# Performance work log

Measured on AMD Instinct MI355X. Metric: run time of the kernel, lower is better.

The kernel has to match this reference:

```python
import jax, jax.numpy as jnp
import numpy as np

IMG = 512
STRIDES = (8.0, 16.0, 32.0)   # p3, p4, p5
ROI = 7                        # roi_size
SR = 2                         # roi_align sampling ratio (fixed; torchvision default -1 is adaptive)
IOU_LOW, IOU_HIGH = 0.4, 0.6   # fg/bg matching thresholds (2nd-stage)
NUM_CLASSES = 20
B, R, M, C = 4, 256, 40, 256


def _make_boxes(key, b, n, max_wh):
    k1, k2 = jax.random.split(key)
    cxy = jax.random.uniform(k1, (b, n, 2), minval=0.0, maxval=float(IMG))
    wh = jax.random.uniform(k2, (b, n, 2), minval=16.0, maxval=float(max_wh))
    x1y1 = jnp.clip(cxy - wh / 2, 0.0, IMG - 1.0)
    x2y2 = jnp.clip(cxy + wh / 2, x1y1 + 1.0, float(IMG))
    return jnp.concatenate([x1y1, x2y2], axis=-1)


def setup_inputs() -> dict:
    key = jax.random.key(0)
    ks = jax.random.split(key, 12)
    feats_p3 = jax.random.normal(ks[0], (B, C, 64, 64), jnp.float32)
    feats_p4 = jax.random.normal(ks[1], (B, C, 32, 32), jnp.float32)
    feats_p5 = jax.random.normal(ks[2], (B, C, 16, 16), jnp.float32)
    props_p3 = _make_boxes(ks[3], B, R, 128)
    props_p4 = _make_boxes(ks[4], B, R, 256)
    props_p5 = _make_boxes(ks[5], B, R, 512)
    gt_xyxy = _make_boxes(ks[6], B, M, 400)
    gt_cls = jax.random.randint(ks[7], (B, M, 1), 0, NUM_CLASSES).astype(jnp.float32)
    gt = jnp.concatenate([gt_xyxy, gt_cls], axis=-1)
    pad = (jnp.arange(M) >= 25)[None, :, None]   # last 15 rows are padding (class -1)
    gt_boxes = jnp.where(pad, -1.0, gt)
    conv_w = jax.random.normal(ks[8], (C, C, 3, 3), jnp.float32) * 0.01
    conv_b = jnp.zeros((C,), jnp.float32)
    fc_w = jax.random.normal(ks[9], (NUM_CLASSES + 1, C * ROI * ROI), jnp.float32) * 0.01
    fc_b = jnp.zeros((NUM_CLASSES + 1,), jnp.float32)
    return {"feats_p3": feats_p3, "feats_p4": feats_p4, "feats_p5": feats_p5,
            "props_p3": props_p3, "props_p4": props_p4, "props_p5": props_p5,
            "gt_boxes": gt_boxes, "conv_w": conv_w, "conv_b": conv_b,
            "fc_w": fc_w, "fc_b": fc_b}


def _bilinear(feat, ys, xs):
    # feat: (C,H,W); ys: (R,G,1); xs: (R,1,G) -> (C,R,G,G)
    Cc, H, W = feat.shape
    valid = (ys >= -1.0) & (ys <= H) & (xs >= -1.0) & (xs <= W)
    y = jnp.clip(ys, 0.0, H - 1.0)
    x = jnp.clip(xs, 0.0, W - 1.0)
    y0f = jnp.floor(y); x0f = jnp.floor(x)
    y0 = y0f.astype(jnp.int32); x0 = x0f.astype(jnp.int32)
    y1 = jnp.minimum(y0 + 1, H - 1); x1 = jnp.minimum(x0 + 1, W - 1)
    ly = y - y0f; lx = x - x0f
    hy = 1.0 - ly; hx = 1.0 - lx
    v = (feat[:, y0, x0] * (hy * hx) + feat[:, y0, x1] * (hy * lx)
         + feat[:, y1, x0] * (ly * hx) + feat[:, y1, x1] * (ly * lx))
    return jnp.where(valid, v, 0.0)


def _roi_align(feat, rois, scale):
    # feat: (C,H,W); rois: (R,4) xyxy in image coords; aligned=True
    r = rois.shape[0]
    x1 = rois[:, 0] * scale - 0.5
    y1 = rois[:, 1] * scale - 0.5
    roi_w = rois[:, 2] * scale - 0.5 - x1
    roi_h = rois[:, 3] * scale - 0.5 - y1
    G = ROI * SR
    frac = (jnp.arange(G, dtype=feat.dtype) + 0.5) / G
    xs = x1[:, None] + frac[None, :] * roi_w[:, None]   # (R,G)
    ys = y1[:, None] + frac[None, :] * roi_h[:, None]
    v = _bilinear(feat, ys[:, :, None], xs[:, None, :])  # (C,R,G,G)
    v = v.transpose(1, 0, 2, 3).reshape(r, -1, ROI, SR, ROI, SR)
    return v.mean(axis=(3, 5))                            # (R,C,7,7)


def _iou(b1, b2):
    # b1: (N,4), b2: (M,4) -> (N,M)
    tl = jnp.maximum(b1[:, None, :2], b2[None, :, :2])
    br = jnp.minimum(b1[:, None, 2:4], b2[None, :, 2:4])
    inter = jnp.clip(br - tl, 0.0).prod(-1)
    a1 = (b1[:, 2:4] - b1[:, :2]).prod(-1)
    a2 = (b2[:, 2:4] - b2[:, :2]).prod(-1)
    return inter / (a1[:, None] + a2[None, :] - inter)


def _match(props, gt):
    # props: (N,4); gt: (M,5) padded with class -1
    valid = gt[:, 4] != -1
    m = jnp.where(valid[None, :], _iou(props, gt[:, :4]), -1.0)
    q = m.max(axis=1)
    matched = gt[m.argmax(axis=1)]                       # (N,5)
    matched = jnp.where((q <= IOU_LOW)[:, None], -1.0, matched)      # background
    matched = jnp.where(((q > IOU_LOW) & (q < IOU_HIGH))[:, None], -1e8, matched)  # neutral
    return matched


def reference(feats_p3, feats_p4, feats_p5, props_p3, props_p4, props_p5,
              gt_boxes, conv_w, conv_b, fc_w, fc_b):
    levels = [(feats_p3, props_p3, STRIDES[0]),
              (feats_p4, props_p4, STRIDES[1]),
              (feats_p5, props_p5, STRIDES[2])]
    # ROI-align every proposal at its level; order: image-major, then level, then roi
    per_level = [jax.vmap(lambda f, p, s=s: _roi_align(f, p, 1.0 / s))(f, p)
                 for f, p, s in levels]                   # each (B,R,C,7,7)
    roi_feats = jnp.stack(per_level, axis=1).reshape(-1, C, ROI, ROI)
    # cls head: conv3x3 + relu + flatten + linear
    h = jax.lax.conv_general_dilated(roi_feats, conv_w, (1, 1), 'SAME')
    h = jax.nn.relu(h + conv_b[None, :, None, None])
    logits = h.reshape(h.shape[0], -1) @ fc_w.T + fc_b    # (B*3*R, num_classes+1)
    # match concatenated per-image proposals to GT (no-grad pipeline)
    props_all = jnp.concatenate([props_p3, props_p4, props_p5], axis=1)  # (B,3R,4)
    matched = jax.vmap(_match)(jax.lax.stop_gradient(props_all), gt_boxes)
    return logits, matched
```

## Files before the change

kernel.cpp:

```cpp
#include <hip/hip_runtime.h>

typedef unsigned short ushort_t;
typedef __attribute__((ext_vector_type(4))) unsigned short ushort4_t;
typedef __attribute__((ext_vector_type(8))) short short8;
typedef __attribute__((ext_vector_type(4))) float floatx4;
typedef __attribute__((ext_vector_type(16))) float floatx16;

#define B_ 4
#define C_ 256
#define R_ 256
#define M_ 40
#define NCLS 21
#define ROI_ 7
#define G_ 14
#define NROI_TOT 3072
#define PROPS_PER_IMG 768
#define POOL_PITCH 264
#define WCONV_ELEMS (256 * 2304)
#define WFC_ELEMS (21 * 12544)
#define OFF_FWB   WCONV_ELEMS
#define OFF_CL3   (OFF_FWB + WFC_ELEMS)
#define OFF_CL4   (OFF_CL3 + 4 * 64 * 64 * 256)
#define OFF_CL5   (OFF_CL4 + 4 * 32 * 32 * 256)

__device__ __forceinline__ ushort_t f2bf(float f) {
  unsigned u = __builtin_bit_cast(unsigned, f);
  u += 0x7fff + ((u >> 16) & 1);
  return (ushort_t)(u >> 16);
}
__device__ __forceinline__ float bf2f(ushort_t h) {
  unsigned u = ((unsigned)h) << 16;
  return __builtin_bit_cast(float, u);
}

__global__ __launch_bounds__(256) void prep_kernel(
    const float* __restrict__ cw, const float* __restrict__ fw,
    const float* __restrict__ f3, const float* __restrict__ f4,
    const float* __restrict__ f5, const float* __restrict__ p3,
    const float* __restrict__ p4, const float* __restrict__ p5,
    const float* __restrict__ gt, ushort_t* __restrict__ wr,
    ushort_t* __restrict__ fwb, ushort_t* __restrict__ cl3,
    ushort_t* __restrict__ cl4, ushort_t* __restrict__ cl5,
    float* __restrict__ out) {
  __shared__ ushort_t tile[64 * 257];
  const int id = blockIdx.x;
  const int t = threadIdx.x;

  if (id < 512) {
    const int i0 = id * 256 + t;
    const int stride = 512 * 256;
    for (int idx = i0; idx < WCONV_ELEMS; idx += stride) {
      const int kk = idx >> 12;
      const int rem = idx & 4095;
      const int co = rem >> 4;
      const int i = rem & 15;
      const int k = kk * 16 + i;
      const int j = k >> 8;
      const int ci = k & 255;
      wr[idx] = f2bf(cw[(co * 256 + ci) * 9 + j]);
    }
    for (int idx = i0; idx < WFC_ELEMS; idx += stride) fwb[idx] = f2bf(fw[idx]);
  } else if (id < 960) {
    const int fid = id - 512;
    const float* in;
    ushort_t* outp;
    int b, y, W;
    if (fid < 256) { in = f3; outp = cl3; W = 64; b = fid >> 6; y = fid & 63; }
    else if (fid < 384) { in = f4; outp = cl4; W = 32; b = (fid - 256) >> 5; y = (fid - 256) & 31; }
    else { in = f5; outp = cl5; W = 16; b = (fid - 384) >> 4; y = (fid - 384) & 15; }

    for (int idx = t; idx < 256 * W; idx += 256) {
      const int c = idx / W;
      const int x = idx - c * W;
      tile[x * 257 + c] = f2bf(in[((size_t)(b * 256 + c) * W + y) * W + x]);
    }
    __syncthreads();
    ushort_t* orow = outp + ((size_t)(b * W + y) * W) * 256;
    for (int idx = t; idx < W * 64; idx += 256) {
      const int x = idx >> 6;
      const int c4 = (idx & 63) * 4;
      ushort4_t v;
      v[0] = tile[x * 257 + c4 + 0];
      v[1] = tile[x * 257 + c4 + 1];
      v[2] = tile[x * 257 + c4 + 2];
      v[3] = tile[x * 257 + c4 + 3];
      *(ushort4_t*)(orow + (size_t)x * 256 + c4) = v;
    }
  } else {
    const int gidx = (id - 960) * 256 + t;
    if (gidx >= NROI_TOT) return;
    const int b = gidx / PROPS_PER_IMG;
    const int i = gidx - b * PROPS_PER_IMG;
    const int lvl = i >> 8;
    const int r = i & 255;
    const float* prop =
        (lvl == 0 ? p3 : (lvl == 1 ? p4 : p5)) + (size_t)(b * R_ + r) * 4;
    const float px1 = prop[0], py1 = prop[1], px2 = prop[2], py2 = prop[3];
    const float a1 = (px2 - px1) * (py2 - py1);
    const float* gtb = gt + (size_t)b * M_ * 5;

    float best = -2.f;
    int bi = 0;
    for (int j = 0; j < M_; ++j) {
      const float gx1 = gtb[j * 5 + 0], gy1 = gtb[j * 5 + 1];
      const float gx2 = gtb[j * 5 + 2], gy2 = gtb[j * 5 + 3];
      const float cls = gtb[j * 5 + 4];
      const float tlx = fmaxf(px1, gx1), tly = fmaxf(py1, gy1);
      const float brx = fminf(px2, gx2), bry = fminf(py2, gy2);
      const float iw = fmaxf(brx - tlx, 0.f), ih = fmaxf(bry - tly, 0.f);
      const float inter = iw * ih;
      const float a2 = (gx2 - gx1) * (gy2 - gy1);
      const float iou = inter / ((a1 + a2) - inter);
      const float m = (cls != -1.0f) ? iou : -1.0f;
      if (m > best) { best = m; bi = j; }
    }
    float o0, o1, o2, o3, o4;
    if (best <= 0.4f) {
      o0 = o1 = o2 = o3 = o4 = -1.0f;
    } else if (best < 0.6f) {
      o0 = o1 = o2 = o3 = o4 = -1e8f;
    } else {
      o0 = gtb[bi * 5 + 0]; o1 = gtb[bi * 5 + 1]; o2 = gtb[bi * 5 + 2];
      o3 = gtb[bi * 5 + 3]; o4 = gtb[bi * 5 + 4];
    }
    float* od = out + (size_t)NROI_TOT * NCLS + (size_t)gidx * 5;
    od[0] = o0; od[1] = o1; od[2] = o2; od[3] = o3; od[4] = o4;
  }
}

__global__ __launch_bounds__(512, 4) void cls_head_kernel(
    const ushort_t* __restrict__ cl3, const ushort_t* __restrict__ cl4,
    const ushort_t* __restrict__ cl5, const float* __restrict__ p3,
    const float* __restrict__ p4, const float* __restrict__ p5,
    const ushort_t* __restrict__ wr, const float* __restrict__ conv_b,
    const ushort_t* __restrict__ fwb, const float* __restrict__ fc_b,
    float* __restrict__ out) {
  __shared__ __align__(16) ushort_t s_pool[2 * 50 * POOL_PITCH];
  __shared__ int s_iy0[28], s_iy1[28], s_ix0[28], s_ix1[28];
  __shared__ float s_ly[28], s_lx[28], s_vy[28], s_vx[28];
  __shared__ float s_fcred[512];

  const int g = blockIdx.x;
  const int t = threadIdx.x;

  const ushort_t* clb_[2];
  int W_[2];
  const float* prop_[2];
#pragma unroll
  for (int rr = 0; rr < 2; ++rr) {
    const int rid = g * 2 + rr;
    const int b = rid / PROPS_PER_IMG;
    const int rem = rid - b * PROPS_PER_IMG;
    const int lvl = rem >> 8;
    const int r = rem & 255;
    const ushort_t* base;
    const float* pp;
    int Wl;
    if (lvl == 0) { base = cl3; pp = p3; Wl = 64; }
    else if (lvl == 1) { base = cl4; pp = p4; Wl = 32; }
    else { base = cl5; pp = p5; Wl = 16; }
    clb_[rr] = base + (size_t)b * Wl * Wl * 256;
    W_[rr] = Wl;
    prop_[rr] = pp + (size_t)(b * R_ + r) * 4;
  }

  if (t < POOL_PITCH) {
    s_pool[49 * POOL_PITCH + t] = 0;
    s_pool[99 * POOL_PITCH + t] = 0;
  }

  if (t < 56) {
    const int rr = t / 28;
    const int tt = t - rr * 28;
    const float* prop = prop_[rr];
    const int H = W_[rr];
    const float scale = 1.0f / (float)(H == 64 ? 8 : (H == 32 ? 16 : 32));
    const float bx1 = prop[0], by1 = prop[1], bx2 = prop[2], by2 = prop[3];
    const float ax = bx1 * scale - 0.5f;
    const float ay = by1 * scale - 0.5f;
    const float rw = bx2 * scale - 0.5f - ax;
    const float rh = by2 * scale - 0.5f - ay;
    const int i = (tt < G_) ? tt : (tt - G_);
    const float frac = ((float)i + 0.5f) / (float)G_;
    const int o = rr * G_ + i;
    if (tt < G_) {
      float yy = ay + frac * rh;
      float v = (yy >= -1.0f && yy <= (float)H) ? 1.0f : 0.0f;
      float y = fminf(fmaxf(yy, 0.0f), (float)(H - 1));
      float y0f = floorf(y);
      int y0 = (int)y0f;
      s_iy0[o] = y0;
      s_iy1[o] = min(y0 + 1, H - 1);
      s_ly[o] = y - y0f;
      s_vy[o] = v;
    } else {
      float xx = ax + frac * rw;
      float v = (xx >= -1.0f && xx <= (float)H) ? 1.0f : 0.0f;
      float x = fminf(fmaxf(xx, 0.0f), (float)(H - 1));
      float x0f = floorf(x);
      int x0 = (int)x0f;
      s_ix0[o] = x0;
      s_ix1[o] = min(x0 + 1, H - 1);
      s_lx[o] = x - x0f;
      s_vx[o] = v;
    }
  }
  __syncthreads();

  const int l = t & 63;
  const int w = t >> 6;

  {
    const int hw = l >> 5;
    const int c8 = (l & 31) * 8;
    for (int cb = w * 2; cb < 98; cb += 16) {
      const int cell = cb + hw;
      if (cell >= 98) continue;
      const int rr = (cell >= 49) ? 1 : 0;
      const int pos = cell - rr * 49;
      const int py = pos / 7, px = pos - (pos / 7) * 7;
      const ushort_t* clb = clb_[rr];
      const int W = W_[rr];
      float a[8];
#pragma unroll
      for (int i = 0; i < 8; ++i) a[i] = 0.f;
#pragma unroll
      for (int sy = 0; sy < 2; ++sy) {
        const int gy = rr * G_ + 2 * py + sy;
        const int iy0 = s_iy0[gy], iy1 = s_iy1[gy];
        const float ly = s_ly[gy], vy = s_vy[gy];
        const float hy = 1.0f - ly;
#pragma unroll
        for (int sx = 0; sx < 2; ++sx) {
          const int gx = rr * G_ + 2 * px + sx;
          const int ix0 = s_ix0[gx], ix1 = s_ix1[gx];
          const float lx = s_lx[gx], vx = s_vx[gx];
          const float hx = 1.0f - lx;
          const float vv = vy * vx;
          const float w00 = vv * hy * hx, w01 = vv * hy * lx;
          const float w10 = vv * ly * hx, w11 = vv * ly * lx;
          const short8 u00 = *(const short8*)(clb + ((size_t)(iy0 * W + ix0) * 256 + c8));
          const short8 u01 = *(const short8*)(clb + ((size_t)(iy0 * W + ix1) * 256 + c8));
          const short8 u10 = *(const short8*)(clb + ((size_t)(iy1 * W + ix0) * 256 + c8));
          const short8 u11 = *(const short8*)(clb + ((size_t)(iy1 * W + ix1) * 256 + c8));
#pragma unroll
          for (int i = 0; i < 8; ++i) {
            a[i] += w00 * bf2f((ushort_t)u00[i]) + w01 * bf2f((ushort_t)u01[i]) +
                    w10 * bf2f((ushort_t)u10[i]) + w11 * bf2f((ushort_t)u11[i]);
          }
        }
      }
      short8 pv;
#pragma unroll
      for (int i = 0; i < 8; ++i) pv[i] = (short)f2bf(a[i] * 0.25f);
      *(short8*)&s_pool[(rr * 50 + pos) * POOL_PITCH + c8] = pv;
    }
  }
  __syncthreads();

  const int ml = l & 31;
  const int quad = l >> 5;
  const int co_base = w * 32;

  const int pA = ml;
  const int pB = ml + 32;
  const int pyA = pA / 7, pxA = pA % 7;
  const int pyB = pB / 7, pxB = pB % 7;

  floatx16 acc[4];
#pragma unroll
  for (int a = 0; a < 4; ++a)
#pragma unroll
    for (int i = 0; i < 16; ++i) acc[a][i] = 0.f;

  const ushort_t* a0p = wr + (co_base + ml) * 16 + quad * 8;

  int kk = 0;
  for (int j = 0; j < 9; ++j) {
    const int dy = j / 3 - 1, dx = j % 3 - 1;
    int bnA, bnB;
    {
      const int ry = pyA + dy, rx = pxA + dx;
      const bool ok = (ry >= 0) & (ry < 7) & (rx >= 0) & (rx < 7);
      bnA = ok ? ry * 7 + rx : 49;
    }
    {
      const int ry = pyB + dy, rx = pxB + dx;
      const bool ok = (pB < 49) & (ry >= 0) & (ry < 7) & (rx >= 0) & (rx < 7);
      bnB = ok ? ry * 7 + rx : 49;
    }
    const int row0 = bnA, row1 = bnB, row2 = 50 + bnA, row3 = 50 + bnB;

#pragma unroll 4
    for (int kc = 0; kc < 16; ++kc, ++kk) {
      const short8 a0 = *(const short8*)(a0p + kk * 4096);
      const int cof = kc * 16 + quad * 8;
      const short8 b0 = *(const short8*)&s_pool[row0 * POOL_PITCH + cof];
      const short8 b1 = *(const short8*)&s_pool[row1 * POOL_PITCH + cof];
      const short8 b2 = *(const short8*)&s_pool[row2 * POOL_PITCH + cof];
      const short8 b3 = *(const short8*)&s_pool[row3 * POOL_PITCH + cof];
      acc[0] = __builtin_amdgcn_mfma_f32_32x32x16_bf16(a0, b0, acc[0], 0, 0, 0);
      acc[1] = __builtin_amdgcn_mfma_f32_32x32x16_bf16(a0, b1, acc[1], 0, 0, 0);
      acc[2] = __builtin_amdgcn_mfma_f32_32x32x16_bf16(a0, b2, acc[2], 0, 0, 0);
      acc[3] = __builtin_amdgcn_mfma_f32_32x32x16_bf16(a0, b3, acc[3], 0, 0, 0);
    }
  }
  __syncthreads();

  ushort_t* h_lds = s_pool;
#pragma unroll
  for (int reg = 0; reg < 16; ++reg) {
    const int co = co_base + (reg & 3) + 8 * (reg >> 2) + 4 * quad;
    const float cb = conv_b[co];
    const int base = co * 49;
    h_lds[base + pA] = f2bf(fmaxf(acc[0][reg] + cb, 0.f));
    h_lds[12544 + base + pA] = f2bf(fmaxf(acc[2][reg] + cb, 0.f));
    if (pB < 49) {
      h_lds[base + pB] = f2bf(fmaxf(acc[1][reg] + cb, 0.f));
      h_lds[12544 + base + pB] = f2bf(fmaxf(acc[3][reg] + cb, 0.f));
    }
  }
  __syncthreads();

  {
    const int n = l & 15;
    const int kq = (l >> 4) * 8;
    const int cls0 = min(n, 20);
    const int cls1 = min(16 + n, 20);
    const ushort_t* ap0 = fwb + (size_t)cls0 * 12544 + kq;
    const ushort_t* ap1 = fwb + (size_t)cls1 * 12544 + kq;
    const ushort_t* bp = h_lds + (size_t)(l & 1) * 12544 + kq;
    const int kbase = w * 1568;

    floatx4 fa0, fa1;
#pragma unroll
    for (int i = 0; i < 4; ++i) { fa0[i] = 0.f; fa1[i] = 0.f; }

    for (int it = 0; it < 49; ++it) {
      const int k = kbase + it * 32;
      const short8 av0 = *(const short8*)(ap0 + k);
      const short8 av1 = *(const short8*)(ap1 + k);
      const short8 bv = *(const short8*)(bp + k);
      fa0 = __builtin_amdgcn_mfma_f32_16x16x32_bf16(av0, bv, fa0, 0, 0, 0);
      fa1 = __builtin_amdgcn_mfma_f32_16x16x32_bf16(av1, bv, fa1, 0, 0, 0);
    }
    if (n < 2) {
      const int m4 = (l >> 4) * 4;
#pragma unroll
      for (int reg = 0; reg < 4; ++reg) {
        s_fcred[((m4 + reg) * 2 + n) * 8 + w] = fa0[reg];
        s_fcred[((16 + m4 + reg) * 2 + n) * 8 + w] = fa1[reg];
      }
    }
  }
  __syncthreads();
  if (t < 2 * NCLS) {
    const int cls = t >> 1;
    const int rr = t & 1;
    const float* pr = &s_fcred[(cls * 2 + rr) * 8];
    float s = pr[0] + pr[1] + pr[2] + pr[3] + pr[4] + pr[5] + pr[6] + pr[7];
    out[(size_t)(g * 2 + rr) * NCLS + cls] = s + fc_b[cls];
  }
}

extern "C" void kernel_launch(void* const* d_in, const int* in_sizes, int n_in,
                              void* d_out, int out_size, void* d_ws,
                              size_t ws_size, hipStream_t stream) {
  const float* f3 = (const float*)d_in[0];
  const float* f4 = (const float*)d_in[1];
  const float* f5 = (const float*)d_in[2];
  const float* p3 = (const float*)d_in[3];
  const float* p4 = (const float*)d_in[4];
  const float* p5 = (const float*)d_in[5];
  const float* gt = (const float*)d_in[6];
  const float* cw = (const float*)d_in[7];
  const float* cb = (const float*)d_in[8];
  const float* fw = (const float*)d_in[9];
  const float* fb = (const float*)d_in[10];
  float* out = (float*)d_out;

  ushort_t* wsp = (ushort_t*)d_ws;
  ushort_t* wr = wsp;
  ushort_t* fwb = wsp + OFF_FWB;
  ushort_t* cl3 = wsp + OFF_CL3;
  ushort_t* cl4 = wsp + OFF_CL4;
  ushort_t* cl5 = wsp + OFF_CL5;

  prep_kernel<<<972, 256, 0, stream>>>(cw, fw, f3, f4, f5, p3, p4, p5, gt, wr,
                                       fwb, cl3, cl4, cl5, out);
  cls_head_kernel<<<NROI_TOT / 2, 512, 0, stream>>>(cl3, cl4, cl5, p3, p4, p5,
                                                    wr, cb, fwb, fb, out);
}
```

Measured before the change: 393.6 us.

## Block-interleave FC weights, swizzle ROI block order, pack bilinear math

```diff
diff --git a/kernel.cpp b/kernel.cpp
--- a/kernel.cpp
+++ b/kernel.cpp
@@ -3,6 +3,8 @@
 typedef unsigned short ushort_t;
 typedef __attribute__((ext_vector_type(4))) unsigned short ushort4_t;
 typedef __attribute__((ext_vector_type(8))) short short8;
+typedef __attribute__((ext_vector_type(4))) unsigned int uint4v;
+typedef __attribute__((ext_vector_type(2))) float float2v;
 typedef __attribute__((ext_vector_type(4))) float floatx4;
 typedef __attribute__((ext_vector_type(16))) float floatx16;
 
@@ -17,9 +19,10 @@
 #define PROPS_PER_IMG 768
 #define POOL_PITCH 264
 #define WCONV_ELEMS (256 * 2304)
-#define WFC_ELEMS (21 * 12544)
+#define NKB 392
+#define WFC2_ELEMS (NKB * 32 * 32)
 #define OFF_FWB   WCONV_ELEMS
-#define OFF_CL3   (OFF_FWB + WFC_ELEMS)
+#define OFF_CL3   (OFF_FWB + WFC2_ELEMS)
 #define OFF_CL4   (OFF_CL3 + 4 * 64 * 64 * 256)
 #define OFF_CL5   (OFF_CL4 + 4 * 32 * 32 * 256)
 
@@ -31,6 +34,12 @@
 __device__ __forceinline__ float bf2f(ushort_t h) {
   unsigned u = ((unsigned)h) << 16;
   return __builtin_bit_cast(float, u);
+}
+__device__ __forceinline__ float2v cvt2(unsigned u) {
+  float2v r;
+  r[0] = __builtin_bit_cast(float, u << 16);
+  r[1] = __builtin_bit_cast(float, u & 0xffff0000u);
+  return r;
 }
 
 __global__ __launch_bounds__(256) void prep_kernel(
@@ -59,7 +68,14 @@
       const int ci = k & 255;
       wr[idx] = f2bf(cw[(co * 256 + ci) * 9 + j]);
     }
-    for (int idx = i0; idx < WFC_ELEMS; idx += stride) fwb[idx] = f2bf(fw[idx]);
+    for (int idx = i0; idx < WFC2_ELEMS; idx += stride) {
+      const int kb = idx >> 10;
+      const int rem = idx & 1023;
+      const int cls = rem >> 5;
+      const int koff = rem & 31;
+      fwb[idx] =
+          (cls < NCLS) ? f2bf(fw[(size_t)cls * 12544 + kb * 32 + koff]) : 0;
+    }
   } else if (id < 960) {
     const int fid = id - 512;
     const float* in;
@@ -140,15 +156,19 @@
   __shared__ float s_ly[28], s_lx[28], s_vy[28], s_vx[28];
   __shared__ float s_fcred[512];
 
-  const int g = blockIdx.x;
+  const int bid = blockIdx.x;
   const int t = threadIdx.x;
+
+  const int img = (bid & 7) >> 1;
+  const int pair = (bid >> 3) * 2 + (bid & 1);
+  const int rid0 = img * PROPS_PER_IMG + pair * 2;
 
   const ushort_t* clb_[2];
   int W_[2];
   const float* prop_[2];
 #pragma unroll
   for (int rr = 0; rr < 2; ++rr) {
-    const int rid = g * 2 + rr;
+    const int rid = rid0 + rr;
     const int b = rid / PROPS_PER_IMG;
     const int rem = rid - b * PROPS_PER_IMG;
     const int lvl = rem >> 8;
@@ -221,9 +241,8 @@
       const int py = pos / 7, px = pos - (pos / 7) * 7;
       const ushort_t* clb = clb_[rr];
       const int W = W_[rr];
-      float a[8];
-#pragma unroll
-      for (int i = 0; i < 8; ++i) a[i] = 0.f;
+      float2v a01 = {0.f, 0.f}, a23 = {0.f, 0.f};
+      float2v a45 = {0.f, 0.f}, a67 = {0.f, 0.f};
 #pragma unroll
       for (int sy = 0; sy < 2; ++sy) {
         const int gy = rr * G_ + 2 * py + sy;
@@ -239,20 +258,29 @@
           const float vv = vy * vx;
           const float w00 = vv * hy * hx, w01 = vv * hy * lx;
           const float w10 = vv * ly * hx, w11 = vv * ly * lx;
-          const short8 u00 = *(const short8*)(clb + ((size_t)(iy0 * W + ix0) * 256 + c8));
-          const short8 u01 = *(const short8*)(clb + ((size_t)(iy0 * W + ix1) * 256 + c8));
-          const short8 u10 = *(const short8*)(clb + ((size_t)(iy1 * W + ix0) * 256 + c8));
-          const short8 u11 = *(const short8*)(clb + ((size_t)(iy1 * W + ix1) * 256 + c8));
-#pragma unroll
-          for (int i = 0; i < 8; ++i) {
-            a[i] += w00 * bf2f((ushort_t)u00[i]) + w01 * bf2f((ushort_t)u01[i]) +
-                    w10 * bf2f((ushort_t)u10[i]) + w11 * bf2f((ushort_t)u11[i]);
-          }
+          const uint4v u00 = *(const uint4v*)(clb + ((size_t)(iy0 * W + ix0) * 256 + c8));
+          const uint4v u01 = *(const uint4v*)(clb + ((size_t)(iy0 * W + ix1) * 256 + c8));
+          const uint4v u10 = *(const uint4v*)(clb + ((size_t)(iy1 * W + ix0) * 256 + c8));
+          const uint4v u11 = *(const uint4v*)(clb + ((size_t)(iy1 * W + ix1) * 256 + c8));
+          a01 += cvt2(u00[0]) * w00 + cvt2(u01[0]) * w01 +
+                 cvt2(u10[0]) * w10 + cvt2(u11[0]) * w11;
+          a23 += cvt2(u00[1]) * w00 + cvt2(u01[1]) * w01 +
+                 cvt2(u10[1]) * w10 + cvt2(u11[1]) * w11;
+          a45 += cvt2(u00[2]) * w00 + cvt2(u01[2]) * w01 +
+                 cvt2(u10[2]) * w10 + cvt2(u11[2]) * w11;
+          a67 += cvt2(u00[3]) * w00 + cvt2(u01[3]) * w01 +
+                 cvt2(u10[3]) * w10 + cvt2(u11[3]) * w11;
         }
       }
       short8 pv;
-#pragma unroll
-      for (int i = 0; i < 8; ++i) pv[i] = (short)f2bf(a[i] * 0.25f);
+      pv[0] = (short)f2bf(a01[0] * 0.25f);
+      pv[1] = (short)f2bf(a01[1] * 0.25f);
+      pv[2] = (short)f2bf(a23[0] * 0.25f);
+      pv[3] = (short)f2bf(a23[1] * 0.25f);
+      pv[4] = (short)f2bf(a45[0] * 0.25f);
+      pv[5] = (short)f2bf(a45[1] * 0.25f);
+      pv[6] = (short)f2bf(a67[0] * 0.25f);
+      pv[7] = (short)f2bf(a67[1] * 0.25f);
       *(short8*)&s_pool[(rr * 50 + pos) * POOL_PITCH + c8] = pv;
     }
   }
@@ -324,28 +352,26 @@
 
   {
     const int n = l & 15;
-    const int kq = (l >> 4) * 8;
-    const int cls0 = min(n, 20);
-    const int cls1 = min(16 + n, 20);
-    const ushort_t* ap0 = fwb + (size_t)cls0 * 12544 + kq;
-    const ushort_t* ap1 = fwb + (size_t)cls1 * 12544 + kq;
-    const ushort_t* bp = h_lds + (size_t)(l & 1) * 12544 + kq;
-    const int kbase = w * 1568;
+    const int kq = l >> 4;
+    const ushort_t* ap0 = fwb + (n * 4 + kq) * 8;
+    const ushort_t* ap1 = ap0 + 512;
+    const ushort_t* bp = h_lds + (size_t)(l & 1) * 12544 + kq * 8;
+    const int kb0 = w * 49;
 
     floatx4 fa0, fa1;
 #pragma unroll
     for (int i = 0; i < 4; ++i) { fa0[i] = 0.f; fa1[i] = 0.f; }
 
     for (int it = 0; it < 49; ++it) {
-      const int k = kbase + it * 32;
-      const short8 av0 = *(const short8*)(ap0 + k);
-      const short8 av1 = *(const short8*)(ap1 + k);
-      const short8 bv = *(const short8*)(bp + k);
+      const int kb = kb0 + it;
+      const short8 av0 = *(const short8*)(ap0 + kb * 1024);
+      const short8 av1 = *(const short8*)(ap1 + kb * 1024);
+      const short8 bv = *(const short8*)(bp + kb * 32);
       fa0 = __builtin_amdgcn_mfma_f32_16x16x32_bf16(av0, bv, fa0, 0, 0, 0);
       fa1 = __builtin_amdgcn_mfma_f32_16x16x32_bf16(av1, bv, fa1, 0, 0, 0);
     }
     if (n < 2) {
-      const int m4 = (l >> 4) * 4;
+      const int m4 = kq * 4;
 #pragma unroll
       for (int reg = 0; reg < 4; ++reg) {
         s_fcred[((m4 + reg) * 2 + n) * 8 + w] = fa0[reg];
@@ -359,7 +385,7 @@
     const int rr = t & 1;
     const float* pr = &s_fcred[(cls * 2 + rr) * 8];
     float s = pr[0] + pr[1] + pr[2] + pr[3] + pr[4] + pr[5] + pr[6] + pr[7];
-    out[(size_t)(g * 2 + rr) * NCLS + cls] = s + fc_b[cls];
+    out[(size_t)(rid0 + rr) * NCLS + cls] = s + fc_b[cls];
   }
 }
 
```

Measured after the change: 368.8 us. -6.3%, faster.
